# Kernel tuning notes

Measured on AMD Instinct MI355X. Metric: run time of the kernel, lower is better.

The kernel has to match this reference:

```python
import jax, jax.numpy as jnp
import numpy as np

TOPK = 2  # config.topk_exp


def setup_inputs() -> dict:
    key = jax.random.key(0)
    ks = jax.random.split(key, 4)
    B, S, D, F, E = 4, 1024, 768, 3072, 8
    scale_in = 1.0 / np.sqrt(D)
    scale_hid = 1.0 / np.sqrt(F)
    return {
        "x": jax.random.normal(ks[0], (B, S, D), dtype=jnp.float32),
        "router_w": jax.random.normal(ks[1], (E, D), dtype=jnp.float32) * scale_in,
        "w_fc": jax.random.normal(ks[2], (E, D, F), dtype=jnp.float32) * scale_in,
        "b_fc": jnp.zeros((E, F), dtype=jnp.float32),
        "w_proj": jax.random.normal(ks[3], (E, F, D), dtype=jnp.float32) * scale_hid,
        "b_proj": jnp.zeros((E, D), dtype=jnp.float32),
    }


def _moe_forward(x, router_w, w_fc, b_fc, w_proj, b_proj):
    B, S, D = x.shape
    E = router_w.shape[0]
    xt = x.reshape(-1, D)  # [T, D] tokens
    # per-token router: Linear(D, E, bias=False)
    gate_logits = xt @ router_w.T  # [T, E]
    # topk_exp > 1: raw logits -> topk -> softmax over the k selected logits
    weights, selected = jax.lax.top_k(gate_logits, TOPK)  # [T, k]
    weights = jax.nn.softmax(weights.astype(jnp.float32), axis=1).astype(x.dtype)
    # combine weights per expert: w[t, e] = sum_k weights[t,k] * (selected[t,k]==e)
    onehot = jax.nn.one_hot(selected, E, dtype=x.dtype)  # [T, k, E]
    comb = jnp.einsum('tk,tke->te', weights, onehot)  # [T, E]
    # expert MLP (GPT-2 style: fc -> gelu -> proj), evaluated densely then combined
    h = jax.nn.gelu(jnp.einsum('td,edf->etf', xt, w_fc) + b_fc[:, None, :], approximate=False)
    y = jnp.einsum('etf,efd->etd', h, w_proj) + b_proj[:, None, :]  # [E, T, D]
    out = jnp.einsum('te,etd->td', comb, y)  # weighted scatter-combine
    return out.reshape(B, S, D)


def reference(x, router_w, w_fc, b_fc, w_proj, b_proj):
    return _moe_forward(x, router_w, w_fc, b_fc, w_proj, b_proj)
```

## Files before the change

kernel.cpp:

```cpp
#include <hip/hip_runtime.h>
#include <hip/hip_bf16.h>

#define TT 4096
#define DD 768
#define FF 3072
#define EE 8
#define NSLOT 8192
#define NSLOT_PAD 8320

#define WAITCNT_VM4 0x0F74
#define WAITCNT_VM7 0x0F77

typedef __attribute__((ext_vector_type(8))) short bf16x8;
typedef __attribute__((ext_vector_type(4))) float f32x4;
typedef const __attribute__((address_space(1))) void* gas1_t;
typedef __attribute__((address_space(3))) void* las3_t;

__global__ __launch_bounds__(256) void router2_kernel(const float* __restrict__ x,
    const float* __restrict__ rw, int* __restrict__ tokE, float* __restrict__ tokW,
    int* __restrict__ blkCnt) {
  __shared__ float rws[EE * 832];
  __shared__ int cnt_s[EE];
  int tid = threadIdx.x;
  if (tid < EE) cnt_s[tid] = 0;
#pragma unroll
  for (int k = 0; k < 6; ++k) {
    int c = tid + k * 256;
    int e = c / 192, rem = c % 192;
    int s = rem / 12, i = rem % 12;
    float4 v = *(const float4*)&rw[e * DD + s * 48 + i * 4];
    *(float4*)&rws[e * 832 + s * 52 + i * 4] = v;
  }
  __syncthreads();
  int lane = tid & 63;
  int sl = lane & 15;
  int t = blockIdx.x * 16 + (tid >> 6) * 4 + (lane >> 4);
  const float4* xp = (const float4*)(x + (size_t)t * DD + sl * 48);
  float acc[EE];
#pragma unroll
  for (int e = 0; e < EE; ++e) acc[e] = 0.f;
#pragma unroll
  for (int i = 0; i < 12; ++i) {
    float4 xv = xp[i];
#pragma unroll
    for (int e = 0; e < EE; ++e) {
      float4 rv = *(const float4*)&rws[e * 832 + sl * 52 + i * 4];
      acc[e] = fmaf(xv.x, rv.x, fmaf(xv.y, rv.y, fmaf(xv.z, rv.z, fmaf(xv.w, rv.w, acc[e]))));
    }
  }
#pragma unroll
  for (int off = 8; off > 0; off >>= 1) {
#pragma unroll
    for (int e = 0; e < EE; ++e) acc[e] += __shfl_xor(acc[e], off);
  }
  if (sl == 0) {
    float v0 = -1e30f; int e0 = 0;
#pragma unroll
    for (int e = 0; e < EE; ++e) { if (acc[e] > v0) { v0 = acc[e]; e0 = e; } }
    float v1 = -1e30f; int e1 = 0;
#pragma unroll
    for (int e = 0; e < EE; ++e) { if (e != e0 && acc[e] > v1) { v1 = acc[e]; e1 = e; } }
    float w1 = 1.f / (1.f + __expf(v0 - v1));
    float w0 = 1.f - w1;
    tokE[2 * t] = e0; tokE[2 * t + 1] = e1;
    tokW[2 * t] = w0; tokW[2 * t + 1] = w1;
    atomicAdd(&cnt_s[e0], 1);
    atomicAdd(&cnt_s[e1], 1);
  }
  __syncthreads();
  if (tid < EE) blkCnt[blockIdx.x * EE + tid] = cnt_s[tid];
}

__global__ __launch_bounds__(256) void offsets2_kernel(const int* __restrict__ blkCnt,
    int* __restrict__ offs, int* __restrict__ blkBase,
    int* __restrict__ tile1, int* __restrict__ tile2, int* __restrict__ meta) {
  __shared__ int wsum[4][EE];
  int tid = threadIdx.x;
  int lane = tid & 63, w = tid >> 6;
  int c[EE], s[EE];
#pragma unroll
  for (int e = 0; e < EE; ++e) { c[e] = blkCnt[tid * EE + e]; s[e] = c[e]; }
#pragma unroll
  for (int off = 1; off < 64; off <<= 1) {
#pragma unroll
    for (int e = 0; e < EE; ++e) {
      int v = __shfl_up(s[e], off);
      if (lane >= off) s[e] += v;
    }
  }
  if (lane == 63) {
#pragma unroll
    for (int e = 0; e < EE; ++e) wsum[w][e] = s[e];
  }
  __syncthreads();
#pragma unroll
  for (int e = 0; e < EE; ++e) {
    int pre = 0;
    for (int w2 = 0; w2 < w; ++w2) pre += wsum[w2][e];
    s[e] += pre;
  }
  int tot[EE];
#pragma unroll
  for (int e = 0; e < EE; ++e) tot[e] = wsum[0][e] + wsum[1][e] + wsum[2][e] + wsum[3][e];
  int offl[EE + 1];
  offl[0] = 0;
#pragma unroll
  for (int e = 0; e < EE; ++e) offl[e + 1] = offl[e] + tot[e];
#pragma unroll
  for (int e = 0; e < EE; ++e) blkBase[tid * EE + e] = offl[e] + s[e] - c[e];
  if (tid == 0) {
    for (int e = 0; e <= EE; ++e) offs[e] = offl[e];
    int n1 = 0, n2 = 0;
    for (int e = 0; e < EE; ++e) { n1 += (tot[e] + 127) / 128; n2 += (tot[e] + 63) / 64; }
    meta[0] = n1; meta[1] = n2;
  }
  if (tid < EE) {
    int p1 = 0, p2 = 0;
    for (int e = 0; e < tid; ++e) { p1 += (tot[e] + 127) / 128; p2 += (tot[e] + 63) / 64; }
    for (int m = 0; m < tot[tid]; m += 128) tile1[p1++] = (tid << 20) | m;
    for (int m = 0; m < tot[tid]; m += 64)  tile2[p2++] = (tid << 20) | m;
  }
}

__global__ __launch_bounds__(256) void scatter_gather2_kernel(const float* __restrict__ x,
    const int* __restrict__ tokE, const float* __restrict__ tokW,
    const int* __restrict__ blkBase, int* __restrict__ slotIdx, float* __restrict__ slotW,
    int* __restrict__ slotTok, __hip_bfloat16* __restrict__ Xg) {
  __shared__ int base_s[EE], lcur[EE];
  __shared__ int sl_s[16][2];
  int tid = threadIdx.x;
  int b = blockIdx.x;
  if (tid < EE) { base_s[tid] = blkBase[b * EE + tid]; lcur[tid] = 0; }
  __syncthreads();
  if (tid < 16) {
    int t = b * 16 + tid;
    int e0 = tokE[2 * t], e1 = tokE[2 * t + 1];
    int s0 = base_s[e0] + atomicAdd(&lcur[e0], 1);
    int s1 = base_s[e1] + atomicAdd(&lcur[e1], 1);
    slotIdx[2 * t] = s0; slotIdx[2 * t + 1] = s1;
    slotW[s0] = tokW[2 * t]; slotW[s1] = tokW[2 * t + 1];
    slotTok[s0] = t; slotTok[s1] = t;
    sl_s[tid][0] = s0; sl_s[tid][1] = s1;
  }
  __syncthreads();
  int k = tid >> 4, p = tid & 15;
  int t = b * 16 + k;
  int s0 = sl_s[k][0], s1 = sl_s[k][1];
  const float4* src = (const float4*)(x + (size_t)t * DD);
  ushort4* d0 = (ushort4*)(Xg + (size_t)s0 * DD);
  ushort4* d1 = (ushort4*)(Xg + (size_t)s1 * DD);
#pragma unroll
  for (int i = 0; i < 12; ++i) {
    int idx = i * 16 + p;
    float4 v = src[idx];
    union { ushort4 u; __hip_bfloat16 h[4]; } cv;
    cv.h[0] = __float2bfloat16(v.x);
    cv.h[1] = __float2bfloat16(v.y);
    cv.h[2] = __float2bfloat16(v.z);
    cv.h[3] = __float2bfloat16(v.w);
    d0[idx] = cv.u;
    d1[idx] = cv.u;
  }
}

__global__ void transpose_convert_kernel(const float* __restrict__ w_fc, __hip_bfloat16* __restrict__ wfcT,
                                         const float* __restrict__ w_proj, __hip_bfloat16* __restrict__ wprojT) {
  __shared__ float tile[64][65];
  int bx = blockIdx.x;
  const float* S; __hip_bfloat16* D; int K, N, n0, k0;
  if (bx < 576) { S = w_fc;   D = wfcT;   K = DD; N = FF; n0 = (bx % 48) * 64; k0 = (bx / 48) * 64; }
  else { bx -= 576; S = w_proj; D = wprojT; K = FF; N = DD; n0 = (bx % 12) * 64; k0 = (bx / 12) * 64; }
  S += (size_t)blockIdx.z * K * N;
  D += (size_t)blockIdx.z * K * N;
  int tid = threadIdx.x;
#pragma unroll
  for (int i = 0; i < 4; ++i) {
    int slot = i * 256 + tid;
    int r = slot >> 4, c4 = slot & 15;
    float4 v = *(const float4*)&S[(size_t)(k0 + r) * N + n0 + c4 * 4];
    tile[r][c4 * 4 + 0] = v.x; tile[r][c4 * 4 + 1] = v.y;
    tile[r][c4 * 4 + 2] = v.z; tile[r][c4 * 4 + 3] = v.w;
  }
  __syncthreads();
#pragma unroll
  for (int i = 0; i < 4; ++i) {
    int slot = i * 256 + tid;
    int n = slot >> 4, kc = slot & 15;
    union { ushort4 u; __hip_bfloat16 h[4]; } cv;
    cv.h[0] = __float2bfloat16(tile[kc * 4 + 0][n]);
    cv.h[1] = __float2bfloat16(tile[kc * 4 + 1][n]);
    cv.h[2] = __float2bfloat16(tile[kc * 4 + 2][n]);
    cv.h[3] = __float2bfloat16(tile[kc * 4 + 3][n]);
    *(ushort4*)&D[(size_t)(n0 + n) * K + k0 + kc * 4] = cv.u;
  }
}

__device__ __forceinline__ float gelu_f(float v) {
  float z = v * 0.70710678118654752f;
  float az = fabsf(z);
  float t = 1.0f / (1.0f + 0.3275911f * az);
  float poly = t * (0.254829592f + t * (-0.284496736f + t * (1.421413741f +
               t * (-1.453152027f + t * 1.061405429f))));
  float erf_abs = 1.0f - poly * __expf(-az * az);
  float erf = copysignf(erf_abs, z);
  return 0.5f * v * (1.0f + erf);
}

__device__ __forceinline__ int swz4(int m) { return (m + (m >> 2)) & 3; }

__global__ __launch_bounds__(256) void gemm1_kernel(const __hip_bfloat16* __restrict__ Xg,
    const __hip_bfloat16* __restrict__ wfcT, const float* __restrict__ b_fc,
    __hip_bfloat16* __restrict__ H, const int* __restrict__ offs,
    const int* __restrict__ tile1, const int* __restrict__ meta) {
  __shared__ __align__(16) short As[2][128 * 32];
  __shared__ __align__(16) short Bs[2][128 * 32];
  if ((int)blockIdx.y >= meta[0]) return;
  int tv = tile1[blockIdx.y];
  int e = tv >> 20;
  int m_base = tv & 0xFFFFF;
  int off_e = offs[e];
  int n_e = offs[e + 1] - off_e;
  int n0 = blockIdx.x * 128;
  const short* A = (const short*)Xg + (size_t)(off_e + m_base) * DD;
  const short* B = (const short*)wfcT + (size_t)e * FF * DD + (size_t)n0 * DD;
  int tid = threadIdx.x;
  int lane = tid & 63, wid = tid >> 6;
  int l15 = lane & 15, q = lane >> 4;
  int wm = wid & 1, wn = wid >> 1;
  int fs0 = tid, fs1 = tid + 256;
  int m0 = fs0 >> 2, c0 = (fs0 & 3) ^ swz4(m0);
  int m1 = fs1 >> 2, c1 = (fs1 & 3) ^ swz4(m1);
  const short* gA0 = A + (size_t)m0 * DD + c0 * 8;
  const short* gA1 = A + (size_t)m1 * DD + c1 * 8;
  const short* gB0 = B + (size_t)m0 * DD + c0 * 8;
  const short* gB1 = B + (size_t)m1 * DD + c1 * 8;
  int aoff[4], boff[4];
#pragma unroll
  for (int mi = 0; mi < 4; ++mi) {
    int r = wm * 64 + mi * 16 + l15;
    aoff[mi] = (r * 4 + (q ^ swz4(r))) * 8;
  }
#pragma unroll
  for (int ni = 0; ni < 4; ++ni) {
    int r = wn * 64 + ni * 16 + l15;
    boff[ni] = (r * 4 + (q ^ swz4(r))) * 8;
  }
  f32x4 acc[4][4] = {};
  __builtin_amdgcn_global_load_lds((gas1_t)gA0, (las3_t)(&As[0][0] + fs0 * 8), 16, 0, 0);
  __builtin_amdgcn_global_load_lds((gas1_t)gA1, (las3_t)(&As[0][0] + fs1 * 8), 16, 0, 0);
  __builtin_amdgcn_global_load_lds((gas1_t)gB0, (las3_t)(&Bs[0][0] + fs0 * 8), 16, 0, 0);
  __builtin_amdgcn_global_load_lds((gas1_t)gB1, (las3_t)(&Bs[0][0] + fs1 * 8), 16, 0, 0);
  gA0 += 32; gA1 += 32; gB0 += 32; gB1 += 32;
  for (int it = 0; it < DD / 32; ++it) {
    int cur = it & 1, nxt = cur ^ 1;
    short* curA = &As[cur][0];
    short* curB = &Bs[cur][0];
    __builtin_amdgcn_s_barrier();
    __builtin_amdgcn_global_load_lds((gas1_t)gA0, (las3_t)(&As[nxt][0] + fs0 * 8), 16, 0, 0);
    __builtin_amdgcn_global_load_lds((gas1_t)gA1, (las3_t)(&As[nxt][0] + fs1 * 8), 16, 0, 0);
    __builtin_amdgcn_global_load_lds((gas1_t)gB0, (las3_t)(&Bs[nxt][0] + fs0 * 8), 16, 0, 0);
    __builtin_amdgcn_global_load_lds((gas1_t)gB1, (las3_t)(&Bs[nxt][0] + fs1 * 8), 16, 0, 0);
    gA0 += 32; gA1 += 32; gB0 += 32; gB1 += 32;
    __builtin_amdgcn_s_waitcnt(WAITCNT_VM4);
    __builtin_amdgcn_s_barrier();
    bf16x8 af[4], bfr[4];
#pragma unroll
    for (int mi = 0; mi < 4; ++mi) af[mi] = *(const bf16x8*)(curA + aoff[mi]);
#pragma unroll
    for (int ni = 0; ni < 4; ++ni) bfr[ni] = *(const bf16x8*)(curB + boff[ni]);
#pragma unroll
    for (int mi = 0; mi < 4; ++mi)
#pragma unroll
      for (int ni = 0; ni < 4; ++ni)
        acc[mi][ni] = __builtin_amdgcn_mfma_f32_16x16x32_bf16(af[mi], bfr[ni], acc[mi][ni], 0, 0, 0);
  }
  float bias[4];
#pragma unroll
  for (int ni = 0; ni < 4; ++ni) bias[ni] = b_fc[e * FF + n0 + wn * 64 + ni * 16 + l15];
  __hip_bfloat16* Hp = H + (size_t)(off_e + m_base) * FF + n0;
#pragma unroll
  for (int mi = 0; mi < 4; ++mi) {
#pragma unroll
    for (int r = 0; r < 4; ++r) {
      int ml = wm * 64 + mi * 16 + q * 4 + r;
      if (m_base + ml < n_e) {
#pragma unroll
        for (int ni = 0; ni < 4; ++ni) {
          int nl = wn * 64 + ni * 16 + l15;
          float v = acc[mi][ni][r] + bias[ni];
          Hp[(size_t)ml * FF + nl] = __float2bfloat16(gelu_f(v));
        }
      }
    }
  }
}

__global__ __launch_bounds__(256) void gemm2_kernel(const __hip_bfloat16* __restrict__ H,
    const __hip_bfloat16* __restrict__ wprojT, const float* __restrict__ b_proj,
    const float* __restrict__ slotW, const int* __restrict__ slotTok,
    float* __restrict__ out, const int* __restrict__ offs,
    const int* __restrict__ tile1, const int* __restrict__ meta) {
  __shared__ __align__(16) short As[2][128 * 32];
  __shared__ __align__(16) short Bs[2][128 * 32];
  if ((int)blockIdx.y >= meta[0]) return;
  int tv = tile1[blockIdx.y];
  int e = tv >> 20;
  int m_base = tv & 0xFFFFF;
  int off_e = offs[e];
  int n_e = offs[e + 1] - off_e;
  int n0 = blockIdx.x * 128;
  int kz = blockIdx.z;
  const short* A = (const short*)H + (size_t)(off_e + m_base) * FF + kz * (FF / 2);
  const short* B = (const short*)wprojT + (size_t)e * DD * FF + (size_t)n0 * FF + kz * (FF / 2);
  int tid = threadIdx.x;
  int lane = tid & 63, wid = tid >> 6;
  int l15 = lane & 15, q = lane >> 4;
  int wm = wid & 1, wn = wid >> 1;
  int fs0 = tid, fs1 = tid + 256;
  int m0 = fs0 >> 2, c0 = (fs0 & 3) ^ swz4(m0);
  int m1 = fs1 >> 2, c1 = (fs1 & 3) ^ swz4(m1);
  const short* gA0 = A + (size_t)m0 * FF + c0 * 8;
  const short* gA1 = A + (size_t)m1 * FF + c1 * 8;
  const short* gB0 = B + (size_t)m0 * FF + c0 * 8;
  const short* gB1 = B + (size_t)m1 * FF + c1 * 8;
  int aoff[4], boff[4];
#pragma unroll
  for (int mi = 0; mi < 4; ++mi) {
    int r = wm * 64 + mi * 16 + l15;
    aoff[mi] = (r * 4 + (q ^ swz4(r))) * 8;
  }
#pragma unroll
  for (int ni = 0; ni < 4; ++ni) {
    int r = wn * 64 + ni * 16 + l15;
    boff[ni] = (r * 4 + (q ^ swz4(r))) * 8;
  }
  f32x4 acc[4][4] = {};
  __builtin_amdgcn_global_load_lds((gas1_t)gA0, (las3_t)(&As[0][0] + fs0 * 8), 16, 0, 0);
  __builtin_amdgcn_global_load_lds((gas1_t)gA1, (las3_t)(&As[0][0] + fs1 * 8), 16, 0, 0);
  __builtin_amdgcn_global_load_lds((gas1_t)gB0, (las3_t)(&Bs[0][0] + fs0 * 8), 16, 0, 0);
  __builtin_amdgcn_global_load_lds((gas1_t)gB1, (las3_t)(&Bs[0][0] + fs1 * 8), 16, 0, 0);
  gA0 += 32; gA1 += 32; gB0 += 32; gB1 += 32;
  for (int it = 0; it < FF / 64; ++it) {
    int cur = it & 1, nxt = cur ^ 1;
    short* curA = &As[cur][0];
    short* curB = &Bs[cur][0];
    __builtin_amdgcn_s_barrier();
    __builtin_amdgcn_global_load_lds((gas1_t)gA0, (las3_t)(&As[nxt][0] + fs0 * 8), 16, 0, 0);
    __builtin_amdgcn_global_load_lds((gas1_t)gA1, (las3_t)(&As[nxt][0] + fs1 * 8), 16, 0, 0);
    __builtin_amdgcn_global_load_lds((gas1_t)gB0, (las3_t)(&Bs[nxt][0] + fs0 * 8), 16, 0, 0);
    __builtin_amdgcn_global_load_lds((gas1_t)gB1, (las3_t)(&Bs[nxt][0] + fs1 * 8), 16, 0, 0);
    gA0 += 32; gA1 += 32; gB0 += 32; gB1 += 32;
    __builtin_amdgcn_s_waitcnt(WAITCNT_VM4);
    __builtin_amdgcn_s_barrier();
    bf16x8 af[4], bfr[4];
#pragma unroll
    for (int mi = 0; mi < 4; ++mi) af[mi] = *(const bf16x8*)(curA + aoff[mi]);
#pragma unroll
    for (int ni = 0; ni < 4; ++ni) bfr[ni] = *(const bf16x8*)(curB + boff[ni]);
#pragma unroll
    for (int mi = 0; mi < 4; ++mi)
#pragma unroll
      for (int ni = 0; ni < 4; ++ni)
        acc[mi][ni] = __builtin_amdgcn_mfma_f32_16x16x32_bf16(af[mi], bfr[ni], acc[mi][ni], 0, 0, 0);
  }
  float bias[4];
#pragma unroll
  for (int ni = 0; ni < 4; ++ni)
    bias[ni] = (kz == 0) ? b_proj[e * DD + n0 + wn * 64 + ni * 16 + l15] : 0.f;
#pragma unroll
  for (int mi = 0; mi < 4; ++mi) {
#pragma unroll
    for (int r = 0; r < 4; ++r) {
      int ml = wm * 64 + mi * 16 + q * 4 + r;
      if (m_base + ml < n_e) {
        int slot = off_e + m_base + ml;
        float w = slotW[slot];
        int tok = slotTok[slot];
        float* op = out + (size_t)tok * DD + n0 + wn * 64;
#pragma unroll
        for (int ni = 0; ni < 4; ++ni)
          atomicAdd(&op[ni * 16 + l15], w * (acc[mi][ni][r] + bias[ni]));
      }
    }
  }
}

extern "C" void kernel_launch(void* const* d_in, const int* in_sizes, int n_in,
                              void* d_out, int out_size, void* d_ws, size_t ws_size,
                              hipStream_t stream) {
  const float* x        = (const float*)d_in[0];
  const float* router_w = (const float*)d_in[1];
  const float* w_fc     = (const float*)d_in[2];
  const float* b_fc     = (const float*)d_in[3];
  const float* w_proj   = (const float*)d_in[4];
  const float* b_proj   = (const float*)d_in[5];
  float* out = (float*)d_out;

  char* p = (char*)d_ws;
  auto alloc = [&](size_t bytes) {
    char* r = p;
    p += (bytes + 255) & ~(size_t)255;
    return r;
  };
  __hip_bfloat16* wfcT   = (__hip_bfloat16*)alloc((size_t)EE * FF * DD * 2);
  __hip_bfloat16* wprojT = (__hip_bfloat16*)alloc((size_t)EE * DD * FF * 2);
  __hip_bfloat16* Xg     = (__hip_bfloat16*)alloc((size_t)NSLOT_PAD * DD * 2);
  __hip_bfloat16* H      = (__hip_bfloat16*)alloc((size_t)NSLOT_PAD * FF * 2);
  int*   tokE    = (int*)alloc(TT * 2 * 4);
  float* tokW    = (float*)alloc(TT * 2 * 4);
  int*   slotIdx = (int*)alloc(TT * 2 * 4);
  float* slotW   = (float*)alloc(NSLOT_PAD * 4);
  int*   slotTok = (int*)alloc(NSLOT_PAD * 4);
  int*   blkCnt  = (int*)alloc(256 * EE * 4);
  int*   blkBase = (int*)alloc(256 * EE * 4);
  int*   tile1   = (int*)alloc(128 * 4);
  int*   tile2   = (int*)alloc(256 * 4);
  int*   offs    = (int*)alloc(64);
  int*   meta    = (int*)alloc(64);

  hipMemsetAsync(out, 0, (size_t)out_size * 4, stream);
  router2_kernel<<<256, 256, 0, stream>>>(x, router_w, tokE, tokW, blkCnt);
  offsets2_kernel<<<1, 256, 0, stream>>>(blkCnt, offs, blkBase, tile1, tile2, meta);
  scatter_gather2_kernel<<<256, 256, 0, stream>>>(x, tokE, tokW, blkBase, slotIdx, slotW, slotTok, Xg);
  transpose_convert_kernel<<<dim3(1152, 1, EE), 256, 0, stream>>>(w_fc, wfcT, w_proj, wprojT);
  gemm1_kernel<<<dim3(FF / 128, 72), 256, 0, stream>>>(Xg, wfcT, b_fc, H, offs, tile1, meta);
  gemm2_kernel<<<dim3(DD / 128, 72, 2), 256, 0, stream>>>(H, wprojT, b_proj, slotW, slotTok, out, offs, tile1, meta);
}
```

Baseline: 417.3 us.

## Triple-buffer GEMM K-loop and remap workgroups across XCDs

Both grouped GEMMs move from a double-buffered K-loop to a three-stage LDS ring with two tiles of loads in flight, using explicit vmcnt/lgkmcnt waits and barriers. The main loop is unrolled by three with static buffer indices and a drain tail. Workgroup IDs are also permuted so consecutive logical tiles land on the same XCD (an interleave by eight), aiming at better L2 reuse of weight and activation tiles. The cost is more LDS per block, which may lower occupancy, and an extra barrier per step.

```diff
diff --git a/kernel.cpp b/kernel.cpp
--- a/kernel.cpp
+++ b/kernel.cpp
@@ -8,8 +8,10 @@
 #define NSLOT 8192
 #define NSLOT_PAD 8320
 
-#define WAITCNT_VM4 0x0F74
-#define WAITCNT_VM7 0x0F77
+#define WVM8  0x0F78
+#define WVM4  0x0F74
+#define WVM0  0x0F70
+#define WLG0  0xC07F
 
 typedef __attribute__((ext_vector_type(8))) short bf16x8;
 typedef __attribute__((ext_vector_type(4))) float f32x4;
@@ -208,19 +210,43 @@
 
 __device__ __forceinline__ int swz4(int m) { return (m + (m >> 2)) & 3; }
 
+#define G_ISSUE(PRE) \
+  __builtin_amdgcn_global_load_lds((gas1_t)gA0, (las3_t)(&As[PRE][0] + fs0 * 8), 16, 0, 0); \
+  __builtin_amdgcn_global_load_lds((gas1_t)gA1, (las3_t)(&As[PRE][0] + fs1 * 8), 16, 0, 0); \
+  __builtin_amdgcn_global_load_lds((gas1_t)gB0, (las3_t)(&Bs[PRE][0] + fs0 * 8), 16, 0, 0); \
+  __builtin_amdgcn_global_load_lds((gas1_t)gB1, (las3_t)(&Bs[PRE][0] + fs1 * 8), 16, 0, 0); \
+  gA0 += 32; gA1 += 32; gB0 += 32; gB1 += 32;
+
+#define G_STEP(CUR, WAITIMM) \
+  __builtin_amdgcn_s_waitcnt(WAITIMM); \
+  __builtin_amdgcn_s_barrier(); \
+  { const short* curA = &As[CUR][0]; const short* curB = &Bs[CUR][0]; \
+    bf16x8 af[4], bfr[4]; \
+    _Pragma("unroll") for (int mi = 0; mi < 4; ++mi) af[mi] = *(const bf16x8*)(curA + aoff[mi]); \
+    _Pragma("unroll") for (int ni = 0; ni < 4; ++ni) bfr[ni] = *(const bf16x8*)(curB + boff[ni]); \
+    _Pragma("unroll") for (int mi = 0; mi < 4; ++mi) \
+      _Pragma("unroll") for (int ni = 0; ni < 4; ++ni) \
+        acc[mi][ni] = __builtin_amdgcn_mfma_f32_16x16x32_bf16(af[mi], bfr[ni], acc[mi][ni], 0, 0, 0); \
+    __builtin_amdgcn_s_waitcnt(WLG0); \
+    __builtin_amdgcn_s_barrier(); }
+
 __global__ __launch_bounds__(256) void gemm1_kernel(const __hip_bfloat16* __restrict__ Xg,
     const __hip_bfloat16* __restrict__ wfcT, const float* __restrict__ b_fc,
     __hip_bfloat16* __restrict__ H, const int* __restrict__ offs,
     const int* __restrict__ tile1, const int* __restrict__ meta) {
-  __shared__ __align__(16) short As[2][128 * 32];
-  __shared__ __align__(16) short Bs[2][128 * 32];
-  if ((int)blockIdx.y >= meta[0]) return;
-  int tv = tile1[blockIdx.y];
+  __shared__ __align__(16) short As[3][128 * 32];
+  __shared__ __align__(16) short Bs[3][128 * 32];
+  int wg = blockIdx.x + 24 * blockIdx.y;
+  int wl = (wg & 7) * 216 + (wg >> 3);
+  int bx = wl % 24;
+  int by = wl / 24;
+  if (by >= meta[0]) return;
+  int tv = tile1[by];
   int e = tv >> 20;
   int m_base = tv & 0xFFFFF;
   int off_e = offs[e];
   int n_e = offs[e + 1] - off_e;
-  int n0 = blockIdx.x * 128;
+  int n0 = bx * 128;
   const short* A = (const short*)Xg + (size_t)(off_e + m_base) * DD;
   const short* B = (const short*)wfcT + (size_t)e * FF * DD + (size_t)n0 * DD;
   int tid = threadIdx.x;
@@ -246,34 +272,16 @@
     boff[ni] = (r * 4 + (q ^ swz4(r))) * 8;
   }
   f32x4 acc[4][4] = {};
-  __builtin_amdgcn_global_load_lds((gas1_t)gA0, (las3_t)(&As[0][0] + fs0 * 8), 16, 0, 0);
-  __builtin_amdgcn_global_load_lds((gas1_t)gA1, (las3_t)(&As[0][0] + fs1 * 8), 16, 0, 0);
-  __builtin_amdgcn_global_load_lds((gas1_t)gB0, (las3_t)(&Bs[0][0] + fs0 * 8), 16, 0, 0);
-  __builtin_amdgcn_global_load_lds((gas1_t)gB1, (las3_t)(&Bs[0][0] + fs1 * 8), 16, 0, 0);
-  gA0 += 32; gA1 += 32; gB0 += 32; gB1 += 32;
-  for (int it = 0; it < DD / 32; ++it) {
-    int cur = it & 1, nxt = cur ^ 1;
-    short* curA = &As[cur][0];
-    short* curB = &Bs[cur][0];
-    __builtin_amdgcn_s_barrier();
-    __builtin_amdgcn_global_load_lds((gas1_t)gA0, (las3_t)(&As[nxt][0] + fs0 * 8), 16, 0, 0);
-    __builtin_amdgcn_global_load_lds((gas1_t)gA1, (las3_t)(&As[nxt][0] + fs1 * 8), 16, 0, 0);
-    __builtin_amdgcn_global_load_lds((gas1_t)gB0, (las3_t)(&Bs[nxt][0] + fs0 * 8), 16, 0, 0);
-    __builtin_amdgcn_global_load_lds((gas1_t)gB1, (las3_t)(&Bs[nxt][0] + fs1 * 8), 16, 0, 0);
-    gA0 += 32; gA1 += 32; gB0 += 32; gB1 += 32;
-    __builtin_amdgcn_s_waitcnt(WAITCNT_VM4);
-    __builtin_amdgcn_s_barrier();
-    bf16x8 af[4], bfr[4];
-#pragma unroll
-    for (int mi = 0; mi < 4; ++mi) af[mi] = *(const bf16x8*)(curA + aoff[mi]);
-#pragma unroll
-    for (int ni = 0; ni < 4; ++ni) bfr[ni] = *(const bf16x8*)(curB + boff[ni]);
-#pragma unroll
-    for (int mi = 0; mi < 4; ++mi)
-#pragma unroll
-      for (int ni = 0; ni < 4; ++ni)
-        acc[mi][ni] = __builtin_amdgcn_mfma_f32_16x16x32_bf16(af[mi], bfr[ni], acc[mi][ni], 0, 0, 0);
-  }
+  G_ISSUE(0)
+  G_ISSUE(1)
+  for (int g = 0; g < 7; ++g) {
+    G_ISSUE(2) G_STEP(0, WVM8)
+    G_ISSUE(0) G_STEP(1, WVM8)
+    G_ISSUE(1) G_STEP(2, WVM8)
+  }
+  G_ISSUE(2) G_STEP(0, WVM8)
+  G_STEP(1, WVM4)
+  G_STEP(2, WVM0)
   float bias[4];
 #pragma unroll
   for (int ni = 0; ni < 4; ++ni) bias[ni] = b_fc[e * FF + n0 + wn * 64 + ni * 16 + l15];
@@ -300,16 +308,21 @@
     const float* __restrict__ slotW, const int* __restrict__ slotTok,
     float* __restrict__ out, const int* __restrict__ offs,
     const int* __restrict__ tile1, const int* __restrict__ meta) {
-  __shared__ __align__(16) short As[2][128 * 32];
-  __shared__ __align__(16) short Bs[2][128 * 32];
-  if ((int)blockIdx.y >= meta[0]) return;
-  int tv = tile1[blockIdx.y];
+  __shared__ __align__(16) short As[3][128 * 32];
+  __shared__ __align__(16) short Bs[3][128 * 32];
+  int wg = blockIdx.x + 6 * blockIdx.y + 432 * blockIdx.z;
+  int wl = (wg & 7) * 108 + (wg >> 3);
+  int bx = wl % 6;
+  int rest = wl / 6;
+  int by = rest % 72;
+  int kz = wl / 432;
+  if (by >= meta[0]) return;
+  int tv = tile1[by];
   int e = tv >> 20;
   int m_base = tv & 0xFFFFF;
   int off_e = offs[e];
   int n_e = offs[e + 1] - off_e;
-  int n0 = blockIdx.x * 128;
-  int kz = blockIdx.z;
+  int n0 = bx * 128;
   const short* A = (const short*)H + (size_t)(off_e + m_base) * FF + kz * (FF / 2);
   const short* B = (const short*)wprojT + (size_t)e * DD * FF + (size_t)n0 * FF + kz * (FF / 2);
   int tid = threadIdx.x;
@@ -335,34 +348,16 @@
     boff[ni] = (r * 4 + (q ^ swz4(r))) * 8;
   }
   f32x4 acc[4][4] = {};
-  __builtin_amdgcn_global_load_lds((gas1_t)gA0, (las3_t)(&As[0][0] + fs0 * 8), 16, 0, 0);
-  __builtin_amdgcn_global_load_lds((gas1_t)gA1, (las3_t)(&As[0][0] + fs1 * 8), 16, 0, 0);
-  __builtin_amdgcn_global_load_lds((gas1_t)gB0, (las3_t)(&Bs[0][0] + fs0 * 8), 16, 0, 0);
-  __builtin_amdgcn_global_load_lds((gas1_t)gB1, (las3_t)(&Bs[0][0] + fs1 * 8), 16, 0, 0);
-  gA0 += 32; gA1 += 32; gB0 += 32; gB1 += 32;
-  for (int it = 0; it < FF / 64; ++it) {
-    int cur = it & 1, nxt = cur ^ 1;
-    short* curA = &As[cur][0];
-    short* curB = &Bs[cur][0];
-    __builtin_amdgcn_s_barrier();
-    __builtin_amdgcn_global_load_lds((gas1_t)gA0, (las3_t)(&As[nxt][0] + fs0 * 8), 16, 0, 0);
-    __builtin_amdgcn_global_load_lds((gas1_t)gA1, (las3_t)(&As[nxt][0] + fs1 * 8), 16, 0, 0);
-    __builtin_amdgcn_global_load_lds((gas1_t)gB0, (las3_t)(&Bs[nxt][0] + fs0 * 8), 16, 0, 0);
-    __builtin_amdgcn_global_load_lds((gas1_t)gB1, (las3_t)(&Bs[nxt][0] + fs1 * 8), 16, 0, 0);
-    gA0 += 32; gA1 += 32; gB0 += 32; gB1 += 32;
-    __builtin_amdgcn_s_waitcnt(WAITCNT_VM4);
-    __builtin_amdgcn_s_barrier();
-    bf16x8 af[4], bfr[4];
-#pragma unroll
-    for (int mi = 0; mi < 4; ++mi) af[mi] = *(const bf16x8*)(curA + aoff[mi]);
-#pragma unroll
-    for (int ni = 0; ni < 4; ++ni) bfr[ni] = *(const bf16x8*)(curB + boff[ni]);
-#pragma unroll
-    for (int mi = 0; mi < 4; ++mi)
-#pragma unroll
-      for (int ni = 0; ni < 4; ++ni)
-        acc[mi][ni] = __builtin_amdgcn_mfma_f32_16x16x32_bf16(af[mi], bfr[ni], acc[mi][ni], 0, 0, 0);
-  }
+  G_ISSUE(0)
+  G_ISSUE(1)
+  for (int g = 0; g < 15; ++g) {
+    G_ISSUE(2) G_STEP(0, WVM8)
+    G_ISSUE(0) G_STEP(1, WVM8)
+    G_ISSUE(1) G_STEP(2, WVM8)
+  }
+  G_ISSUE(2) G_STEP(0, WVM8)
+  G_STEP(1, WVM4)
+  G_STEP(2, WVM0)
   float bias[4];
 #pragma unroll
   for (int ni = 0; ni < 4; ++ni)
@@ -423,6 +418,6 @@
   offsets2_kernel<<<1, 256, 0, stream>>>(blkCnt, offs, blkBase, tile1, tile2, meta);
   scatter_gather2_kernel<<<256, 256, 0, stream>>>(x, tokE, tokW, blkBase, slotIdx, slotW, slotTok, Xg);
   transpose_convert_kernel<<<dim3(1152, 1, EE), 256, 0, stream>>>(w_fc, wfcT, w_proj, wprojT);
-  gemm1_kernel<<<dim3(FF / 128, 72), 256, 0, stream>>>(Xg, wfcT, b_fc, H, offs, tile1, meta);
-  gemm2_kernel<<<dim3(DD / 128, 72, 2), 256, 0, stream>>>(H, wprojT, b_proj, slotW, slotTok, out, offs, tile1, meta);
-}
+  gemm1_kernel<<<dim3(24, 72), 256, 0, stream>>>(Xg, wfcT, b_fc, H, offs, tile1, meta);
+  gemm2_kernel<<<dim3(6, 72, 2), 256, 0, stream>>>(H, wprojT, b_proj, slotW, slotTok, out, offs, tile1, meta);
+}
```

Result: faster. 387.8 us (-7.1%).
